# Kernel tuning notes

Measured on AMD Instinct MI355X. Metric: run time of the kernel, lower is better.

Reference implementation:

```python
import jax, jax.numpy as jnp
import numpy as np

N = 100_000   # num_nodes
D = 64        # emb_dim
E = 1_600_000 # num edges (before self loops)
L = 3         # n_layers
NEG_SLOPE = 0.2


def setup_inputs() -> dict:
    key = jax.random.key(0)
    ks = jax.random.split(key, 6)
    edge_index = jax.random.randint(ks[0], (2, E), 0, N, dtype=jnp.int32)
    # xavier-ish init for embedding and per-layer GATConv params
    emb = jax.random.normal(ks[1], (N, D), jnp.float32) * (1.0 / np.sqrt(D))
    W = jax.random.normal(ks[2], (L, D, D), jnp.float32) * (1.0 / np.sqrt(D))
    att_src = jax.random.normal(ks[3], (L, D), jnp.float32) * 0.1
    att_dst = jax.random.normal(ks[4], (L, D), jnp.float32) * 0.1
    bias = jnp.zeros((L, D), jnp.float32)
    return {"edge_index": edge_index, "emb": emb, "W": W,
            "att_src": att_src, "att_dst": att_dst, "bias": bias}


def _gat_layer(x, src, dst, W, a_s, a_d, b):
    # PyG GATConv, heads=1, concat=False, self-loops already in (src, dst)
    h = x @ W                                   # [N, D]
    e_s = h @ a_s                               # [N] per-node src score
    e_d = h @ a_d                               # [N] per-node dst score
    e = jax.nn.leaky_relu(e_s[src] + e_d[dst], NEG_SLOPE)   # [E']
    # segment softmax grouped by destination node (max is detached in PyG)
    m = jax.lax.stop_gradient(jax.ops.segment_max(e, dst, num_segments=N))
    ex = jnp.exp(e - m[dst])
    denom = jax.ops.segment_sum(ex, dst, num_segments=N)
    alpha = ex / (denom[dst] + 1e-16)           # [E']
    out = jax.ops.segment_sum(alpha[:, None] * h[src], dst, num_segments=N)
    return out + b


def reference(edge_index, emb, W, att_src, att_dst, bias):
    loops = jnp.arange(N, dtype=edge_index.dtype)
    src = jnp.concatenate([edge_index[0], loops])
    dst = jnp.concatenate([edge_index[1], loops])
    x = emb
    outs = [x]
    for l in range(L):
        x = jax.nn.elu(_gat_layer(x, src, dst, W[l], att_src[l], att_dst[l], bias[l]))
        outs.append(x)
    return jnp.mean(jnp.stack(outs, axis=0), axis=0)  # [N, D]
```

## Files before the change

kernel.cpp:

```cpp
#include <hip/hip_runtime.h>
#include <hip/hip_bf16.h>


#define BSHIFT 9
#define NPB 512
#define COL_CAP 10240
#define FRAG_STRIDE 5120
#define CHUNK 4096

typedef _Float16 v8h __attribute__((ext_vector_type(8)));
typedef float v4f __attribute__((ext_vector_type(4)));
typedef unsigned short u16x8 __attribute__((ext_vector_type(8)));

__device__ inline float bf2f(unsigned short u) {
    return __uint_as_float(((unsigned int)u) << 16);
}
__device__ inline unsigned short f2bf(float v) {
    __hip_bfloat16 b = __float2bfloat16(v);
    return *reinterpret_cast<unsigned short*>(&b);
}
__device__ inline unsigned short f2h_u(float v) {
    return __builtin_bit_cast(unsigned short, (_Float16)v);
}
__device__ inline float h2f_u(unsigned short u) {
    return (float)__builtin_bit_cast(_Float16, u);
}

__global__ __launch_bounds__(256) void detect_bf16_k(const unsigned int* raw, int* flag) {
    __shared__ int sc;
    if (threadIdx.x == 0) sc = 0;
    __syncthreads();
    int c = 0;
    for (int i = threadIdx.x; i < 4096; i += 256) {
        unsigned int b = (raw[i] >> 8) & 0x7Fu;
        if (b >= 0x3Bu && b <= 0x3Fu) c++;
    }
    atomicAdd(&sc, c);
    __syncthreads();
    if (threadIdx.x == 0) *flag = (sc > 2048) ? 1 : 0;
}

__device__ inline float load_in(const void* p, int i, int isbf) {
    if (isbf) return bf2f(((const unsigned short*)p)[i]);
    return ((const float*)p)[i];
}

__global__ __launch_bounds__(256) void conv_k(const void* emb, const void* W, const void* as_,
                                              const void* ad_, const void* b_, unsigned short* x0,
                                              unsigned short* Whf, float* bf, int n, int L_,
                                              const int* flag) {
    int i = blockIdx.x * 256 + threadIdx.x;
    int isbf = *flag;
    if (i < n) x0[i] = f2h_u(load_in(emb, i, isbf));
    if (i < L_ * 4096) {
        int l = i >> 12, rem = i & 4095;
        int k = rem >> 6, c64 = rem & 63;
        int t = c64 >> 4, c = c64 & 15;
        int kf = k >> 5, quad = (k >> 3) & 3, j = k & 7;
        int f = t * 2 + kf, lane = quad * 16 + c;
        Whf[l * FRAG_STRIDE + (f * 64 + lane) * 8 + j] = f2h_u(load_in(W, i, isbf));
    }
    if (i < L_ * 1024) {
        int l = i >> 10, r = i & 1023;
        int kf = r >> 9, rr = r & 511;
        int lane = rr >> 3, j = rr & 7;
        int c = lane & 15, quad = lane >> 4;
        int k = kf * 32 + quad * 8 + j;
        float val = 0.f;
        if (c < 2) {
            const void* av = c ? ad_ : as_;
            float dot = 0.f;
            for (int cc = 0; cc < 64; ++cc)
                dot += load_in(W, l * 4096 + k * 64 + cc, isbf) * load_in(av, l * 64 + cc, isbf);
            val = dot;
        }
        Whf[l * FRAG_STRIDE + ((8 + kf) * 64 + lane) * 8 + j] = f2h_u(val);
    }
    if (i < L_ * 64) bf[i] = load_in(b_, i, isbf);
}


__global__ __launch_bounds__(256) void hist_k(const int* __restrict__ dst, int* __restrict__ bh,
                                              int E, int nchunk) {
    __shared__ int h[256];
    h[threadIdx.x] = 0;
    __syncthreads();
    int cs = blockIdx.x * CHUNK;
    int ce = min(cs + CHUNK, E);
    for (int i = cs + threadIdx.x; i < ce; i += 256)
        atomicAdd(&h[dst[i] >> BSHIFT], 1);
    __syncthreads();
    bh[threadIdx.x * nchunk + blockIdx.x] = h[threadIdx.x];
}

__global__ __launch_bounds__(256) void scanb_k(int* __restrict__ bh, int* __restrict__ ghist,
                                               int nchunk) {
    __shared__ int s[256];
    int b = blockIdx.x, t = threadIdx.x;
    int i0 = 2 * t, i1 = 2 * t + 1;
    int v0 = (i0 < nchunk) ? bh[b * nchunk + i0] : 0;
    int v1 = (i1 < nchunk) ? bh[b * nchunk + i1] : 0;
    int p = v0 + v1;
    s[t] = p;
    __syncthreads();
    for (int off = 1; off < 256; off <<= 1) {
        int tv = (t >= off) ? s[t - off] : 0;
        __syncthreads();
        s[t] += tv;
        __syncthreads();
    }
    int excl = s[t] - p;
    if (i0 < nchunk) bh[b * nchunk + i0] = excl;
    if (i1 < nchunk) bh[b * nchunk + i1] = excl + v0;
    if (t == 255) ghist[b] = s[255];
}

__global__ __launch_bounds__(256) void scan_nb_k(const int* ghist, int* pairs_base, int* col_base,
                                                 int* rowptr, int N, int E, int NB) {
    __shared__ int s1[256], s2[256];
    int t = threadIdx.x;
    int hv = (t < NB) ? ghist[t] : 0;
    int npb = (t < NB) ? min(N - (t << BSHIFT), NPB) : 0;
    s1[t] = hv; s2[t] = hv + npb;
    __syncthreads();
    for (int off = 1; off < 256; off <<= 1) {
        int t1 = (t >= off) ? s1[t - off] : 0;
        int t2 = (t >= off) ? s2[t - off] : 0;
        __syncthreads();
        s1[t] += t1; s2[t] += t2;
        __syncthreads();
    }
    if (t < NB) {
        pairs_base[t] = s1[t] - hv;
        col_base[t]   = s2[t] - (hv + npb);
    }
    if (t == 0) rowptr[N] = E + N;
}

__global__ __launch_bounds__(256) void partition_k(const int* __restrict__ src,
                                                   const int* __restrict__ dst,
                                                   const int* __restrict__ bh,
                                                   const int* __restrict__ pairs_base,
                                                   uint2* __restrict__ pairs,
                                                   int E, int NB, int nchunk) {
    __shared__ int base[256], rk[256];
    int t = threadIdx.x;
    base[t] = (t < NB) ? pairs_base[t] + bh[t * nchunk + blockIdx.x] : 0;
    rk[t] = 0;
    __syncthreads();
    int cs = blockIdx.x * CHUNK;
    int ce = min(cs + CHUNK, E);
    for (int i = cs + t; i < ce; i += 256) {
        int d = dst[i];
        int b = d >> BSHIFT;
        int r = atomicAdd(&rk[b], 1);
        pairs[base[b] + r] = make_uint2((unsigned)src[i], (unsigned)d);
    }
}

__global__ __launch_bounds__(512) void build_k(const uint2* __restrict__ pairs,
                                               const int* __restrict__ ghist,
                                               const int* __restrict__ pairs_base,
                                               const int* __restrict__ col_base,
                                               int* __restrict__ rowptr, int* __restrict__ col,
                                               int N) {
    __shared__ int cnt[512], cnt2[512], sc[512], off[513];
    __shared__ int col_lds[COL_CAP];
    int b = blockIdx.x, t = threadIdx.x;
    int nloc = min(N - (b << BSHIFT), NPB);
    int ne = ghist[b], pb = pairs_base[b], cb = col_base[b];
    cnt[t] = 0; cnt2[t] = 0;
    __syncthreads();
    for (int i = t; i < ne; i += 512)
        atomicAdd(&cnt[pairs[pb + i].y & (NPB - 1)], 1);
    __syncthreads();
    int v = cnt[t] + (t < nloc ? 1 : 0);
    sc[t] = v;
    __syncthreads();
    for (int o = 1; o < 512; o <<= 1) {
        int tv = (t >= o) ? sc[t - o] : 0;
        __syncthreads();
        sc[t] += tv;
        __syncthreads();
    }
    off[t + 1] = sc[t];
    if (t == 0) off[0] = 0;
    __syncthreads();
    if (t < nloc) rowptr[(b << BSHIFT) + t] = cb + off[t];
    int total = off[nloc];
    bool fit = (total <= COL_CAP);
    for (int i = t; i < ne; i += 512) {
        uint2 p = pairs[pb + i];
        int loc = p.y & (NPB - 1);
        int pos = off[loc] + atomicAdd(&cnt2[loc], 1);
        if (fit) col_lds[pos] = (int)p.x;
        else     col[cb + pos] = (int)p.x;
    }
    if (t < nloc) {
        int pos = off[t + 1] - 1;
        int sv = (b << BSHIFT) + t;
        if (fit) col_lds[pos] = sv;
        else     col[cb + pos] = sv;
    }
    __syncthreads();
    if (fit)
        for (int i = t; i < total; i += 512) col[cb + i] = col_lds[i];
}


__global__ __launch_bounds__(256) void gemm_k(const unsigned short* __restrict__ x,
                                              const unsigned short* __restrict__ Whf,
                                              unsigned short* __restrict__ h,
                                              float* __restrict__ es, float* __restrict__ ed,
                                              int n, int nblk, int nwaves) {
    int lane = threadIdx.x & 63;
    int gwave = (blockIdx.x * 256 + threadIdx.x) >> 6;
    int c = lane & 15, quad = lane >> 4;

    v8h bfr[10];
    #pragma unroll
    for (int f = 0; f < 10; ++f)
        bfr[f] = *(const v8h*)(Whf + (size_t)(f * 64 + lane) * 8);

    v4f z = {0.f, 0.f, 0.f, 0.f};
    for (int nb = gwave; nb < nblk; nb += nwaves) {
        int base = nb * 16;
        int m = base + c; if (m >= n) m = n - 1;
        const v8h a0 = *(const v8h*)(x + (size_t)m * 64 + quad * 8);
        const v8h a1 = *(const v8h*)(x + (size_t)m * 64 + 32 + quad * 8);
        v4f acc[5];
        #pragma unroll
        for (int t = 0; t < 5; ++t) {
            acc[t] = __builtin_amdgcn_mfma_f32_16x16x32_f16(a0, bfr[2 * t], z, 0, 0, 0);
            acc[t] = __builtin_amdgcn_mfma_f32_16x16x32_f16(a1, bfr[2 * t + 1], acc[t], 0, 0, 0);
        }
        #pragma unroll
        for (int r = 0; r < 4; ++r) {
            int row = base + quad * 4 + r;
            if (row < n) {
                #pragma unroll
                for (int t = 0; t < 4; ++t)
                    h[(size_t)row * 64 + t * 16 + c] = f2h_u(acc[t][r]);
                if (c == 0) es[row] = acc[4][r];
                if (c == 1) ed[row] = acc[4][r];
            }
        }
    }
}

__device__ inline float elu_f(float v) { return v > 0.f ? v : (__expf(v) - 1.f); }

__global__ __launch_bounds__(256) void agg_k(const unsigned short* __restrict__ h,
                                             const float* __restrict__ es,
                                             const float* __restrict__ ed, const int* __restrict__ rowptr,
                                             const int* __restrict__ col, const float* __restrict__ bias,
                                             unsigned short* __restrict__ xo,
                                             const unsigned short* __restrict__ x0,
                                             const unsigned short* __restrict__ x1,
                                             const unsigned short* __restrict__ x2,
                                             void* __restrict__ out, const int* __restrict__ flag,
                                             int write_out, int n) {
    int gw = (blockIdx.x * 256 + threadIdx.x) >> 6;
    int lane = threadIdx.x & 63;
    if (gw >= n) return;
    int start = rowptr[gw], end = rowptr[gw + 1];
    int deg = end - start;
    float edd = ed[gw];

    if (deg <= 64) {
        int c = 0;
        float e = -1e30f;
        if (lane < deg) {
            c = col[start + lane];
            float t = es[c] + edd;
            e = t > 0.f ? t : 0.2f * t;
        }
        float m = e;
        #pragma unroll
        for (int off = 32; off; off >>= 1) m = fmaxf(m, __shfl_xor(m, off));
        float ex = (lane < deg) ? __expf(e - m) : 0.f;
        float sum = ex;
        #pragma unroll
        for (int off = 32; off; off >>= 1) sum += __shfl_xor(sum, off);
        float a = ex / (sum + 1e-16f);

        int g = lane >> 3, j = lane & 7;
        float acc[8];
        #pragma unroll
        for (int i = 0; i < 8; ++i) acc[i] = 0.f;
        for (int t = 0; t < deg; t += 16) {
            int i0 = t + g, i1 = t + 8 + g;
            int   s0  = __shfl(c, i0), s1 = __shfl(c, i1);
            float al0 = __shfl(a, i0), al1 = __shfl(a, i1);
            bool p0 = i0 < deg, p1 = i1 < deg;
            u16x8 hv0, hv1;
            if (p0) hv0 = *(const u16x8*)(h + (size_t)s0 * 64 + j * 8);
            if (p1) hv1 = *(const u16x8*)(h + (size_t)s1 * 64 + j * 8);
            if (p0) {
                #pragma unroll
                for (int i = 0; i < 8; ++i) acc[i] = fmaf(al0, h2f_u(hv0[i]), acc[i]);
            }
            if (p1) {
                #pragma unroll
                for (int i = 0; i < 8; ++i) acc[i] = fmaf(al1, h2f_u(hv1[i]), acc[i]);
            }
        }
        #pragma unroll
        for (int off = 8; off < 64; off <<= 1)
            #pragma unroll
            for (int i = 0; i < 8; ++i)
                acc[i] += __shfl_xor(acc[i], off);

        if (g == 0) {
            size_t base = (size_t)gw * 64 + j * 8;
            float y[8];
            #pragma unroll
            for (int i = 0; i < 8; ++i)
                y[i] = elu_f(acc[i] + bias[j * 8 + i]);
            if (write_out) {
                u16x8 a0v = *(const u16x8*)(x0 + base);
                u16x8 a1v = *(const u16x8*)(x1 + base);
                u16x8 a2v = *(const u16x8*)(x2 + base);
                float v[8];
                #pragma unroll
                for (int i = 0; i < 8; ++i)
                    v[i] = (h2f_u(a0v[i]) + h2f_u(a1v[i]) + h2f_u(a2v[i]) + y[i]) * 0.25f;
                if (*flag) {
                    u16x8 o;
                    #pragma unroll
                    for (int i = 0; i < 8; ++i) o[i] = f2bf(v[i]);
                    *(u16x8*)((unsigned short*)out + base) = o;
                } else {
                    float4 o0 = make_float4(v[0], v[1], v[2], v[3]);
                    float4 o1 = make_float4(v[4], v[5], v[6], v[7]);
                    *(float4*)((float*)out + base) = o0;
                    *(float4*)((float*)out + base + 4) = o1;
                }
            } else {
                u16x8 o;
                #pragma unroll
                for (int i = 0; i < 8; ++i) o[i] = f2h_u(y[i]);
                *(u16x8*)(xo + base) = o;
            }
        }
    } else {
        float m = -1e30f;
        for (int k = start + lane; k < end; k += 64) {
            float e = es[col[k]] + edd;
            e = e > 0.f ? e : 0.2f * e;
            m = fmaxf(m, e);
        }
        #pragma unroll
        for (int off = 32; off; off >>= 1) m = fmaxf(m, __shfl_xor(m, off));
        float sum = 0.f;
        for (int k = start + lane; k < end; k += 64) {
            float e = es[col[k]] + edd;
            e = e > 0.f ? e : 0.2f * e;
            sum += __expf(e - m);
        }
        #pragma unroll
        for (int off = 32; off; off >>= 1) sum += __shfl_xor(sum, off);
        float inv = 1.f / (sum + 1e-16f);
        float acc = 0.f;
        for (int k = start; k < end; ++k) {
            int s = col[k];
            float e = es[s] + edd;
            e = e > 0.f ? e : 0.2f * e;
            float al = __expf(e - m) * inv;
            acc = fmaf(al, h2f_u(h[(size_t)s * 64 + lane]), acc);
        }
        size_t base = (size_t)gw * 64 + lane;
        float y = elu_f(acc + bias[lane]);
        if (write_out) {
            float v = (h2f_u(x0[base]) + h2f_u(x1[base]) + h2f_u(x2[base]) + y) * 0.25f;
            if (*flag) ((unsigned short*)out)[base] = f2bf(v);
            else       ((float*)out)[base] = v;
        } else {
            xo[base] = f2h_u(y);
        }
    }
}


extern "C" void kernel_launch(void* const* d_in, const int* in_sizes, int n_in,
                              void* d_out, int out_size, void* d_ws, size_t ws_size,
                              hipStream_t stream) {
    const int*  edge = (const int*)d_in[0];
    const void* emb  = d_in[1];
    const void* W    = d_in[2];
    const void* as_  = d_in[3];
    const void* ad_  = d_in[4];
    const void* b_   = d_in[5];

    const int E = in_sizes[0] / 2;
    const int N = in_sizes[1] / 64;
    const int L = in_sizes[2] / 4096;
    const int NB = (N + NPB - 1) >> BSHIFT;
    const int nchunk = (E + CHUNK - 1) / CHUNK;
    const size_t N64 = (size_t)N * 64;

    char* p = (char*)d_ws;
    auto take = [&](size_t bytes) { char* r = p; p += (bytes + 255) & ~(size_t)255; return r; };
    unsigned short* x0 = (unsigned short*)take(N64 * 2);
    unsigned short* x1 = (unsigned short*)take(N64 * 2);
    unsigned short* x3 = (unsigned short*)take(N64 * 2);
    unsigned short* h  = (unsigned short*)take(N64 * 2);
    uint2* pairs   = (uint2*)take((size_t)E * 8 > N64 * 2 ? (size_t)E * 8 : N64 * 2);
    unsigned short* x2 = (unsigned short*)pairs;
    float* es      = (float*)take((size_t)N * 4);
    float* ed      = (float*)take((size_t)N * 4);
    unsigned short* Whf = (unsigned short*)take((size_t)L * FRAG_STRIDE * 2);
    float* bf      = (float*)take((size_t)L * 64 * 4);
    int* rowptr    = (int*)take((size_t)(N + 1) * 4);
    int* col       = (int*)take((size_t)(E + N) * 4);
    int* bh        = (int*)take((size_t)256 * 512 * 4);
    int* ghist     = (int*)take(256 * 4);
    int* pairs_base= (int*)take(256 * 4);
    int* col_base  = (int*)take(256 * 4);
    int* flag      = (int*)take(4);

    const int* srcp = edge;
    const int* dstp = edge + E;

    detect_bf16_k<<<1, 256, 0, stream>>>((const unsigned int*)emb, flag);
    conv_k<<<(int)((N64 + 255) / 256), 256, 0, stream>>>(emb, W, as_, ad_, b_, x0, Whf, bf,
                                                         (int)N64, L, flag);

    hist_k<<<nchunk, 256, 0, stream>>>(dstp, bh, E, nchunk);
    scanb_k<<<NB, 256, 0, stream>>>(bh, ghist, nchunk);
    scan_nb_k<<<1, 256, 0, stream>>>(ghist, pairs_base, col_base, rowptr, N, E, NB);
    partition_k<<<nchunk, 256, 0, stream>>>(srcp, dstp, bh, pairs_base, pairs, E, NB, nchunk);
    build_k<<<NB, 512, 0, stream>>>(pairs, ghist, pairs_base, col_base, rowptr, col, N);

    const int nblk = (N + 15) / 16;
    const int ggrid = 512;
    unsigned short* xs[4] = {x0, x1, x2, x3};
    for (int l = 0; l < L; ++l) {
        gemm_k<<<ggrid, 256, 0, stream>>>(xs[l], Whf + (size_t)l * FRAG_STRIDE,
                                          h, es, ed, N, nblk, ggrid * 4);
        agg_k<<<(N + 3) / 4, 256, 0, stream>>>(h, es, ed, rowptr, col, bf + l * 64, xs[l + 1],
                                               x0, x1, x2, d_out, flag,
                                               (l == L - 1) ? 1 : 0, N);
    }
}
```

Measured before the change: 353.8 us.

## Fuse setup kernels, pack edge pairs, aggregate two nodes per wavefront

```diff
diff --git a/kernel.cpp b/kernel.cpp
--- a/kernel.cpp
+++ b/kernel.cpp
@@ -6,7 +6,7 @@
 #define NPB 512
 #define COL_CAP 10240
 #define FRAG_STRIDE 5120
-#define CHUNK 4096
+#define CHUNK 8192
 
 typedef _Float16 v8h __attribute__((ext_vector_type(8)));
 typedef float v4f __attribute__((ext_vector_type(4)));
@@ -26,31 +26,43 @@
     return (float)__builtin_bit_cast(_Float16, u);
 }
 
-__global__ __launch_bounds__(256) void detect_bf16_k(const unsigned int* raw, int* flag) {
-    __shared__ int sc;
-    if (threadIdx.x == 0) sc = 0;
-    __syncthreads();
-    int c = 0;
-    for (int i = threadIdx.x; i < 4096; i += 256) {
-        unsigned int b = (raw[i] >> 8) & 0x7Fu;
-        if (b >= 0x3Bu && b <= 0x3Fu) c++;
-    }
-    atomicAdd(&sc, c);
-    __syncthreads();
-    if (threadIdx.x == 0) *flag = (sc > 2048) ? 1 : 0;
-}
-
 __device__ inline float load_in(const void* p, int i, int isbf) {
     if (isbf) return bf2f(((const unsigned short*)p)[i]);
     return ((const float*)p)[i];
 }
 
-__global__ __launch_bounds__(256) void conv_k(const void* emb, const void* W, const void* as_,
-                                              const void* ad_, const void* b_, unsigned short* x0,
-                                              unsigned short* Whf, float* bf, int n, int L_,
-                                              const int* flag) {
-    int i = blockIdx.x * 256 + threadIdx.x;
-    int isbf = *flag;
+__device__ inline int detect_bf16_blk(const unsigned int* raw) {
+    __shared__ int s4[4];
+    unsigned int b = (raw[threadIdx.x] >> 8) & 0x7Fu;
+    unsigned long long m = __ballot(b >= 0x3Bu && b <= 0x3Fu);
+    int wv = threadIdx.x >> 6;
+    if ((threadIdx.x & 63) == 0) s4[wv] = __popcll(m);
+    __syncthreads();
+    return (s4[0] + s4[1] + s4[2] + s4[3]) > 128 ? 1 : 0;
+}
+
+__global__ __launch_bounds__(256) void conv_hist_k(const void* emb, const void* W, const void* as_,
+                                                   const void* ad_, const void* b_,
+                                                   const int* __restrict__ dst,
+                                                   unsigned short* x0, unsigned short* Whf,
+                                                   float* bf, int* __restrict__ bh, int* flag,
+                                                   int n, int L_, int E, int nchunk) {
+    int blk = blockIdx.x;
+    if (blk < nchunk) {
+        __shared__ int h[256];
+        h[threadIdx.x] = 0;
+        __syncthreads();
+        int cs = blk * CHUNK;
+        int ce = min(cs + CHUNK, E);
+        for (int i = cs + threadIdx.x; i < ce; i += 256)
+            atomicAdd(&h[dst[i] >> BSHIFT], 1);
+        __syncthreads();
+        bh[threadIdx.x * nchunk + blk] = h[threadIdx.x];
+        return;
+    }
+    int isbf = detect_bf16_blk((const unsigned int*)emb);
+    int i = (blk - nchunk) * 256 + threadIdx.x;
+    if (blk == nchunk && threadIdx.x == 0) *flag = isbf;
     if (i < n) x0[i] = f2h_u(load_in(emb, i, isbf));
     if (i < L_ * 4096) {
         int l = i >> 12, rem = i & 4095;
@@ -80,19 +92,6 @@
 }
 
 
-__global__ __launch_bounds__(256) void hist_k(const int* __restrict__ dst, int* __restrict__ bh,
-                                              int E, int nchunk) {
-    __shared__ int h[256];
-    h[threadIdx.x] = 0;
-    __syncthreads();
-    int cs = blockIdx.x * CHUNK;
-    int ce = min(cs + CHUNK, E);
-    for (int i = cs + threadIdx.x; i < ce; i += 256)
-        atomicAdd(&h[dst[i] >> BSHIFT], 1);
-    __syncthreads();
-    bh[threadIdx.x * nchunk + blockIdx.x] = h[threadIdx.x];
-}
-
 __global__ __launch_bounds__(256) void scanb_k(int* __restrict__ bh, int* __restrict__ ghist,
                                                int nchunk) {
     __shared__ int s[256];
@@ -141,7 +140,7 @@
                                                    const int* __restrict__ dst,
                                                    const int* __restrict__ bh,
                                                    const int* __restrict__ pairs_base,
-                                                   uint2* __restrict__ pairs,
+                                                   unsigned int* __restrict__ pairs,
                                                    int E, int NB, int nchunk) {
     __shared__ int base[256], rk[256];
     int t = threadIdx.x;
@@ -154,11 +153,11 @@
         int d = dst[i];
         int b = d >> BSHIFT;
         int r = atomicAdd(&rk[b], 1);
-        pairs[base[b] + r] = make_uint2((unsigned)src[i], (unsigned)d);
-    }
-}
-
-__global__ __launch_bounds__(512) void build_k(const uint2* __restrict__ pairs,
+        pairs[base[b] + r] = (unsigned)src[i] | ((unsigned)(d & (NPB - 1)) << 23);
+    }
+}
+
+__global__ __launch_bounds__(512) void build_k(const unsigned int* __restrict__ pairs,
                                                const int* __restrict__ ghist,
                                                const int* __restrict__ pairs_base,
                                                const int* __restrict__ col_base,
@@ -172,7 +171,7 @@
     cnt[t] = 0; cnt2[t] = 0;
     __syncthreads();
     for (int i = t; i < ne; i += 512)
-        atomicAdd(&cnt[pairs[pb + i].y & (NPB - 1)], 1);
+        atomicAdd(&cnt[pairs[pb + i] >> 23], 1);
     __syncthreads();
     int v = cnt[t] + (t < nloc ? 1 : 0);
     sc[t] = v;
@@ -190,11 +189,12 @@
     int total = off[nloc];
     bool fit = (total <= COL_CAP);
     for (int i = t; i < ne; i += 512) {
-        uint2 p = pairs[pb + i];
-        int loc = p.y & (NPB - 1);
+        unsigned int p = pairs[pb + i];
+        int loc = p >> 23;
         int pos = off[loc] + atomicAdd(&cnt2[loc], 1);
-        if (fit) col_lds[pos] = (int)p.x;
-        else     col[cb + pos] = (int)p.x;
+        int sv = (int)(p & 0x7FFFFFu);
+        if (fit) col_lds[pos] = sv;
+        else     col[cb + pos] = sv;
     }
     if (t < nloc) {
         int pos = off[t + 1] - 1;
@@ -260,123 +260,159 @@
                                              const unsigned short* __restrict__ x2,
                                              void* __restrict__ out, const int* __restrict__ flag,
                                              int write_out, int n) {
-    int gw = (blockIdx.x * 256 + threadIdx.x) >> 6;
+    int wv = (blockIdx.x * 256 + threadIdx.x) >> 6;
     int lane = threadIdx.x & 63;
-    if (gw >= n) return;
-    int start = rowptr[gw], end = rowptr[gw + 1];
-    int deg = end - start;
-    float edd = ed[gw];
-
-    if (deg <= 64) {
+    int n0 = wv * 2;
+    if (n0 >= n) return;
+    int half = lane >> 5, hl = lane & 31;
+    int node = n0 + half;
+    bool valid = node < n;
+    int nodeC = valid ? node : n - 1;
+    int r0 = rowptr[nodeC];
+    int deg = valid ? (rowptr[nodeC + 1] - r0) : 0;
+
+    if (__ballot(deg > 32) == 0) {
+        float edd = valid ? ed[nodeC] : 0.f;
         int c = 0;
-        float e = -1e30f;
-        if (lane < deg) {
-            c = col[start + lane];
-            float t = es[c] + edd;
-            e = t > 0.f ? t : 0.2f * t;
-        }
-        float m = e;
-        #pragma unroll
-        for (int off = 32; off; off >>= 1) m = fmaxf(m, __shfl_xor(m, off));
-        float ex = (lane < deg) ? __expf(e - m) : 0.f;
+        float ex = 0.f;
+        if (hl < deg) {
+            c = col[r0 + hl];
+            float t = es[(unsigned)c] + edd;
+            t = t > 0.f ? t : 0.2f * t;
+            ex = __expf(t);
+        }
         float sum = ex;
         #pragma unroll
-        for (int off = 32; off; off >>= 1) sum += __shfl_xor(sum, off);
+        for (int off = 1; off < 32; off <<= 1) sum += __shfl_xor(sum, off);
         float a = ex / (sum + 1e-16f);
 
+        int deg0 = __shfl(deg, 0), deg1 = __shfl(deg, 32);
         int g = lane >> 3, j = lane & 7;
-        float acc[8];
+        unsigned joff = (unsigned)j * 8;
+        float acc0[8], acc1[8];
         #pragma unroll
-        for (int i = 0; i < 8; ++i) acc[i] = 0.f;
-        for (int t = 0; t < deg; t += 16) {
+        for (int i = 0; i < 8; ++i) { acc0[i] = 0.f; acc1[i] = 0.f; }
+
+        for (int t = 0; t < deg0; t += 16) {
             int i0 = t + g, i1 = t + 8 + g;
             int   s0  = __shfl(c, i0), s1 = __shfl(c, i1);
             float al0 = __shfl(a, i0), al1 = __shfl(a, i1);
-            bool p0 = i0 < deg, p1 = i1 < deg;
+            bool p0 = i0 < deg0, p1 = i1 < deg0;
             u16x8 hv0, hv1;
-            if (p0) hv0 = *(const u16x8*)(h + (size_t)s0 * 64 + j * 8);
-            if (p1) hv1 = *(const u16x8*)(h + (size_t)s1 * 64 + j * 8);
+            if (p0) hv0 = *(const u16x8*)(h + ((unsigned)s0 * 64u + joff));
+            if (p1) hv1 = *(const u16x8*)(h + ((unsigned)s1 * 64u + joff));
             if (p0) {
                 #pragma unroll
-                for (int i = 0; i < 8; ++i) acc[i] = fmaf(al0, h2f_u(hv0[i]), acc[i]);
+                for (int i = 0; i < 8; ++i) acc0[i] = fmaf(al0, h2f_u(hv0[i]), acc0[i]);
             }
             if (p1) {
                 #pragma unroll
-                for (int i = 0; i < 8; ++i) acc[i] = fmaf(al1, h2f_u(hv1[i]), acc[i]);
+                for (int i = 0; i < 8; ++i) acc0[i] = fmaf(al1, h2f_u(hv1[i]), acc0[i]);
+            }
+        }
+        for (int t = 0; t < deg1; t += 16) {
+            int i0 = t + g, i1 = t + 8 + g;
+            int   s0  = __shfl(c, 32 + i0), s1 = __shfl(c, 32 + i1);
+            float al0 = __shfl(a, 32 + i0), al1 = __shfl(a, 32 + i1);
+            bool p0 = i0 < deg1, p1 = i1 < deg1;
+            u16x8 hv0, hv1;
+            if (p0) hv0 = *(const u16x8*)(h + ((unsigned)s0 * 64u + joff));
+            if (p1) hv1 = *(const u16x8*)(h + ((unsigned)s1 * 64u + joff));
+            if (p0) {
+                #pragma unroll
+                for (int i = 0; i < 8; ++i) acc1[i] = fmaf(al0, h2f_u(hv0[i]), acc1[i]);
+            }
+            if (p1) {
+                #pragma unroll
+                for (int i = 0; i < 8; ++i) acc1[i] = fmaf(al1, h2f_u(hv1[i]), acc1[i]);
             }
         }
         #pragma unroll
         for (int off = 8; off < 64; off <<= 1)
             #pragma unroll
-            for (int i = 0; i < 8; ++i)
-                acc[i] += __shfl_xor(acc[i], off);
-
-        if (g == 0) {
-            size_t base = (size_t)gw * 64 + j * 8;
-            float y[8];
-            #pragma unroll
-            for (int i = 0; i < 8; ++i)
-                y[i] = elu_f(acc[i] + bias[j * 8 + i]);
-            if (write_out) {
-                u16x8 a0v = *(const u16x8*)(x0 + base);
-                u16x8 a1v = *(const u16x8*)(x1 + base);
-                u16x8 a2v = *(const u16x8*)(x2 + base);
-                float v[8];
-                #pragma unroll
-                for (int i = 0; i < 8; ++i)
-                    v[i] = (h2f_u(a0v[i]) + h2f_u(a1v[i]) + h2f_u(a2v[i]) + y[i]) * 0.25f;
-                if (*flag) {
+            for (int i = 0; i < 8; ++i) {
+                acc0[i] += __shfl_xor(acc0[i], off);
+                acc1[i] += __shfl_xor(acc1[i], off);
+            }
+
+        if (g < 2) {
+            int wnode = n0 + g;
+            if (wnode < n) {
+                size_t base = (size_t)wnode * 64 + joff;
+                float y[8];
+                #pragma unroll
+                for (int i = 0; i < 8; ++i) {
+                    float v = g ? acc1[i] : acc0[i];
+                    y[i] = elu_f(v + bias[j * 8 + i]);
+                }
+                if (write_out) {
+                    u16x8 a0v = *(const u16x8*)(x0 + base);
+                    u16x8 a1v = *(const u16x8*)(x1 + base);
+                    u16x8 a2v = *(const u16x8*)(x2 + base);
+                    float v[8];
+                    #pragma unroll
+                    for (int i = 0; i < 8; ++i)
+                        v[i] = (h2f_u(a0v[i]) + h2f_u(a1v[i]) + h2f_u(a2v[i]) + y[i]) * 0.25f;
+                    if (*flag) {
+                        u16x8 o;
+                        #pragma unroll
+                        for (int i = 0; i < 8; ++i) o[i] = f2bf(v[i]);
+                        *(u16x8*)((unsigned short*)out + base) = o;
+                    } else {
+                        float4 o0 = make_float4(v[0], v[1], v[2], v[3]);
+                        float4 o1 = make_float4(v[4], v[5], v[6], v[7]);
+                        *(float4*)((float*)out + base) = o0;
+                        *(float4*)((float*)out + base + 4) = o1;
+                    }
+                } else {
                     u16x8 o;
                     #pragma unroll
-                    for (int i = 0; i < 8; ++i) o[i] = f2bf(v[i]);
-                    *(u16x8*)((unsigned short*)out + base) = o;
-                } else {
-                    float4 o0 = make_float4(v[0], v[1], v[2], v[3]);
-                    float4 o1 = make_float4(v[4], v[5], v[6], v[7]);
-                    *(float4*)((float*)out + base) = o0;
-                    *(float4*)((float*)out + base + 4) = o1;
+                    for (int i = 0; i < 8; ++i) o[i] = f2h_u(y[i]);
+                    *(u16x8*)(xo + base) = o;
                 }
+            }
+        }
+    } else {
+        for (int k = 0; k < 2; ++k) {
+            int nk = n0 + k;
+            if (nk >= n) break;
+            int start = __shfl(r0, k * 32);
+            int end = start + __shfl(deg, k * 32);
+            float edd = ed[nk];
+            float m = -1e30f;
+            for (int kk = start + lane; kk < end; kk += 64) {
+                float e = es[col[kk]] + edd;
+                e = e > 0.f ? e : 0.2f * e;
+                m = fmaxf(m, e);
+            }
+            #pragma unroll
+            for (int off = 32; off; off >>= 1) m = fmaxf(m, __shfl_xor(m, off));
+            float sum = 0.f;
+            for (int kk = start + lane; kk < end; kk += 64) {
+                float e = es[col[kk]] + edd;
+                e = e > 0.f ? e : 0.2f * e;
+                sum += __expf(e - m);
+            }
+            #pragma unroll
+            for (int off = 32; off; off >>= 1) sum += __shfl_xor(sum, off);
+            float inv = 1.f / (sum + 1e-16f);
+            float acc = 0.f;
+            for (int kk = start; kk < end; ++kk) {
+                int s = col[kk];
+                float e = es[s] + edd;
+                e = e > 0.f ? e : 0.2f * e;
+                float al = __expf(e - m) * inv;
+                acc = fmaf(al, h2f_u(h[(size_t)s * 64 + lane]), acc);
+            }
+            size_t base = (size_t)nk * 64 + lane;
+            float y = elu_f(acc + bias[lane]);
+            if (write_out) {
+                float v = (h2f_u(x0[base]) + h2f_u(x1[base]) + h2f_u(x2[base]) + y) * 0.25f;
+                if (*flag) ((unsigned short*)out)[base] = f2bf(v);
+                else       ((float*)out)[base] = v;
             } else {
-                u16x8 o;
-                #pragma unroll
-                for (int i = 0; i < 8; ++i) o[i] = f2h_u(y[i]);
-                *(u16x8*)(xo + base) = o;
-            }
-        }
-    } else {
-        float m = -1e30f;
-        for (int k = start + lane; k < end; k += 64) {
-            float e = es[col[k]] + edd;
-            e = e > 0.f ? e : 0.2f * e;
-            m = fmaxf(m, e);
-        }
-        #pragma unroll
-        for (int off = 32; off; off >>= 1) m = fmaxf(m, __shfl_xor(m, off));
-        float sum = 0.f;
-        for (int k = start + lane; k < end; k += 64) {
-            float e = es[col[k]] + edd;
-            e = e > 0.f ? e : 0.2f * e;
-            sum += __expf(e - m);
-        }
-        #pragma unroll
-        for (int off = 32; off; off >>= 1) sum += __shfl_xor(sum, off);
-        float inv = 1.f / (sum + 1e-16f);
-        float acc = 0.f;
-        for (int k = start; k < end; ++k) {
-            int s = col[k];
-            float e = es[s] + edd;
-            e = e > 0.f ? e : 0.2f * e;
-            float al = __expf(e - m) * inv;
-            acc = fmaf(al, h2f_u(h[(size_t)s * 64 + lane]), acc);
-        }
-        size_t base = (size_t)gw * 64 + lane;
-        float y = elu_f(acc + bias[lane]);
-        if (write_out) {
-            float v = (h2f_u(x0[base]) + h2f_u(x1[base]) + h2f_u(x2[base]) + y) * 0.25f;
-            if (*flag) ((unsigned short*)out)[base] = f2bf(v);
-            else       ((float*)out)[base] = v;
-        } else {
-            xo[base] = f2h_u(y);
+                xo[base] = f2h_u(y);
+            }
         }
     }
 }
@@ -405,7 +441,7 @@
     unsigned short* x1 = (unsigned short*)take(N64 * 2);
     unsigned short* x3 = (unsigned short*)take(N64 * 2);
     unsigned short* h  = (unsigned short*)take(N64 * 2);
-    uint2* pairs   = (uint2*)take((size_t)E * 8 > N64 * 2 ? (size_t)E * 8 : N64 * 2);
+    unsigned int* pairs = (unsigned int*)take((size_t)E * 4 > N64 * 2 ? (size_t)E * 4 : N64 * 2);
     unsigned short* x2 = (unsigned short*)pairs;
     float* es      = (float*)take((size_t)N * 4);
     float* ed      = (float*)take((size_t)N * 4);
@@ -421,12 +457,10 @@
 
     const int* srcp = edge;
     const int* dstp = edge + E;
-
-    detect_bf16_k<<<1, 256, 0, stream>>>((const unsigned int*)emb, flag);
-    conv_k<<<(int)((N64 + 255) / 256), 256, 0, stream>>>(emb, W, as_, ad_, b_, x0, Whf, bf,
-                                                         (int)N64, L, flag);
-
-    hist_k<<<nchunk, 256, 0, stream>>>(dstp, bh, E, nchunk);
+    const int convblocks = (int)((N64 + 255) / 256);
+
+    conv_hist_k<<<nchunk + convblocks, 256, 0, stream>>>(emb, W, as_, ad_, b_, dstp, x0, Whf, bf,
+                                                         bh, flag, (int)N64, L, E, nchunk);
     scanb_k<<<NB, 256, 0, stream>>>(bh, ghist, nchunk);
     scan_nb_k<<<1, 256, 0, stream>>>(ghist, pairs_base, col_base, rowptr, N, E, NB);
     partition_k<<<nchunk, 256, 0, stream>>>(srcp, dstp, bh, pairs_base, pairs, E, NB, nchunk);
@@ -434,12 +468,13 @@
 
     const int nblk = (N + 15) / 16;
     const int ggrid = 512;
+    const int aggblocks = (N + 7) / 8;
     unsigned short* xs[4] = {x0, x1, x2, x3};
     for (int l = 0; l < L; ++l) {
         gemm_k<<<ggrid, 256, 0, stream>>>(xs[l], Whf + (size_t)l * FRAG_STRIDE,
                                           h, es, ed, N, nblk, ggrid * 4);
-        agg_k<<<(N + 3) / 4, 256, 0, stream>>>(h, es, ed, rowptr, col, bf + l * 64, xs[l + 1],
-                                               x0, x1, x2, d_out, flag,
-                                               (l == L - 1) ? 1 : 0, N);
-    }
-}
+        agg_k<<<aggblocks, 256, 0, stream>>>(h, es, ed, rowptr, col, bf + l * 64,
+                                             xs[l + 1], x0, x1, x2, d_out, flag,
+                                             (l == L - 1) ? 1 : 0, N);
+    }
+}
```

Result: faster. 346.0 us (-2.2%).
